# Performance work log

Measured on AMD Instinct MI355X. Metric: run time of the kernel, lower is better.

Reference implementation:

```python
import jax, jax.numpy as jnp
import numpy as np

W = 8          # window_size (small/key side)
WU = 2 * W     # window_size_up (big/query side)
H = 4          # num_heads
SF = 128       # sf_dim
BF = 256       # bf_dim
HD = SF // H   # head_dim = 32
SCALE = HD ** -0.5
TABLE = (2 * WU - 1) * (2 * W - 1)  # 465


def _relative_position_index():
    # big coords (2, WU*WU), small coords (2, W*W), 'ij' meshgrid like torch
    ch, cw = jnp.meshgrid(jnp.arange(WU), jnp.arange(WU), indexing='ij')
    big = jnp.stack([ch.reshape(-1), cw.reshape(-1)])          # (2, Nb)
    sh, sw = jnp.meshgrid(jnp.arange(W), jnp.arange(W), indexing='ij')
    small = jnp.stack([sh.reshape(-1), sw.reshape(-1)])        # (2, Ns)
    rel = big[:, :, None] - small[:, None, :]                  # (2, Nb, Ns)
    idx = (rel[0] + W - 1) * (2 * W - 1) + (rel[1] + W - 1)    # (Nb, Ns)
    return idx


def setup_inputs() -> dict:
    key = jax.random.key(0)
    ks = jax.random.split(key, 9)
    B_ = 1024
    Nb, Ns = WU * WU, W * W
    inp = {
        'big_x': jax.random.normal(ks[0], (B_, Nb, BF), jnp.float32),
        'small_x': jax.random.normal(ks[1], (B_, Ns, SF), jnp.float32),
        # proj1: bf_dim -> sf_dim
        'W1': jax.random.normal(ks[2], (BF, SF), jnp.float32) * (BF ** -0.5),
        'b1': jnp.zeros((SF,), jnp.float32),
        # fused qkv: sf_dim -> 3*sf_dim
        'Wqkv': jax.random.normal(ks[3], (SF, 3 * SF), jnp.float32) * (SF ** -0.5),
        'bqkv': jnp.zeros((3 * SF,), jnp.float32),
        # proj2: sf_dim -> bf_dim
        'W2': jax.random.normal(ks[4], (SF, BF), jnp.float32) * (SF ** -0.5),
        'b2': jnp.zeros((BF,), jnp.float32),
        # relative position bias table, trunc_normal std=0.02
        'bias_table': jax.random.normal(ks[5], (TABLE, H), jnp.float32) * 0.02,
    }
    return inp


def reference(big_x, small_x, W1, b1, Wqkv, bqkv, W2, b2, bias_table):
    B_, Nb, _ = big_x.shape
    Ns = small_x.shape[1]

    big = big_x @ W1 + b1                                      # (B, Nb, SF)

    # only q of big and k,v of small are used downstream
    qb = (big @ Wqkv[:, :SF] + bqkv[:SF]).reshape(B_, Nb, H, HD)
    ks_ = (small_x @ Wqkv[:, SF:2 * SF] + bqkv[SF:2 * SF]).reshape(B_, Ns, H, HD)
    vs = (small_x @ Wqkv[:, 2 * SF:] + bqkv[2 * SF:]).reshape(B_, Ns, H, HD)

    attn = jnp.einsum('bqhd,bkhd->bhqk', qb * SCALE, ks_)      # (B, H, Nb, Ns)

    idx = _relative_position_index()                           # (Nb, Ns)
    bias = bias_table[idx]                                     # (Nb, Ns, H)
    attn = attn + jnp.transpose(bias, (2, 0, 1))[None]         # broadcast over B

    attn = jax.nn.softmax(attn, axis=-1)
    out = jnp.einsum('bhqk,bkhd->bqhd', attn, vs).reshape(B_, Nb, SF)
    return out @ W2 + b2                                       # (B, Nb, BF)
```

## Files before the change

kernel.cpp:

```cpp
#include <hip/hip_runtime.h>
#include <stdint.h>

#define NH      4
#define SF      128
#define BF      256
#define HD      32
#define NB      256
#define NS      64
#define NBATCH  1024

typedef short bf16x8 __attribute__((ext_vector_type(8)));
typedef float f32x4  __attribute__((ext_vector_type(4)));

#define WEFFT_OFF 0
#define BEFF_OFF  65536
#define WKVT_OFF  66048
#define W2T_OFF   131584
#define BMATT_OFF 197120

#define LDS_SK  0
#define LDS_SVT 16384
#define LDS_SQ  32768
#define LDS_TOTAL 65536

__device__ __forceinline__ short f2b(float x){
  uint32_t u = __float_as_uint(x);
  u += 0x7fff + ((u >> 16) & 1);
  return (short)(u >> 16);
}
__device__ __forceinline__ uint32_t cvt_pk_bf16(float lo, float hi){
  uint32_t r;
  asm("v_cvt_pk_bf16_f32 %0, %1, %2" : "=v"(r) : "v"(lo), "v"(hi));
  return r;
}
__device__ __forceinline__ int swz256(int row, int byteInRow){
  return row * 256 + (byteInRow ^ ((row & 7) << 4));
}
__device__ __forceinline__ int swz128(int row, int byteInRow){
  return row * 128 + (byteInRow ^ ((row & 7) << 4));
}

__global__ void cowin_prep(const float* __restrict__ W1, const float* __restrict__ b1,
                           const float* __restrict__ Wqkv, const float* __restrict__ bqkv,
                           const float* __restrict__ W2, const float* __restrict__ tbl,
                           void* ws)
{
  short* weffT = (short*)((char*)ws + WEFFT_OFF);
  float* beff  = (float*)((char*)ws + BEFF_OFF);
  short* wkvT  = (short*)((char*)ws + WKVT_OFF);
  short* w2T   = (short*)((char*)ws + W2T_OFF);
  float* bmatT = (float*)((char*)ws + BMATT_OFF);
  const float L2E = 1.4426950408889634f;
  const float QS  = 0.17677669529663687f * L2E;

  int bid = blockIdx.x, t = threadIdx.x;
  if (bid < 128){
    int n = bid, k = t;
    float acc = 0.f;
    for (int c = 0; c < SF; ++c) acc += W1[k * SF + c] * Wqkv[c * (3*SF) + n];
    weffT[n * 256 + k] = f2b(acc * QS);
  } else if (bid == 128){
    if (t < 128){
      int n = t;
      float acc = bqkv[n];
      for (int c = 0; c < SF; ++c) acc += b1[c] * Wqkv[c * (3*SF) + n];
      beff[n] = acc * QS;
    }
  } else if (bid < 145){
    int base = (bid - 129) * 2048 + t * 8;
    for (int j = 0; j < 8; ++j){
      int i = base + j, n = i >> 7, k = i & 127;
      wkvT[i] = f2b(Wqkv[k * (3*SF) + SF + n]);
    }
  } else if (bid < 161){
    int base = (bid - 145) * 2048 + t * 8;
    for (int j = 0; j < 8; ++j){
      int i = base + j, n = i >> 7, k = i & 127;
      w2T[i] = f2b(W2[k * BF + n]);
    }
  } else {
    int i = (bid - 161) * 256 + t;
    int h = i >> 14, kk = (i >> 8) & 63, q = i & 255;
    int qh = q >> 4, qw = q & 15, kh = kk >> 3, kw = kk & 7;
    int idx = (qh - kh + 7) * 15 + (qw - kw + 7);
    bmatT[i] = tbl[idx * 4 + h] * L2E;
  }
}

__global__ __launch_bounds__(512, 4) void cowin_main(
    const float* __restrict__ big_x, const float* __restrict__ small_x,
    const float* __restrict__ bqkv,  const float* __restrict__ b2,
    const void* __restrict__ ws, float* __restrict__ out)
{
  extern __shared__ char smem[];
  const short* weffT = (const short*)((const char*)ws + WEFFT_OFF);
  const float* beff  = (const float*)((const char*)ws + BEFF_OFF);
  const short* wkvT  = (const short*)((const char*)ws + WKVT_OFF);
  const short* w2T   = (const short*)((const char*)ws + W2T_OFF);
  const float* bmatT = (const float*)((const char*)ws + BMATT_OFF);

  const int bid = blockIdx.x;
  const int b  = bid >> 1;
  const int hf = bid & 1;
  const int t    = threadIdx.x;
  const int w    = t >> 6;
  const int lane = t & 63;
  const int li   = lane & 15;
  const int g    = lane >> 4;

  const f32x4 vzero = {0.f, 0.f, 0.f, 0.f};

  const float* bx = big_x + (size_t)b * NB * BF + (size_t)hf * 128 * BF;
  const int qrow = t >> 2, qq = (t & 3) * 16;

  float4 ld[4];
  {
    const float* sx = small_x + (size_t)b * (NS * SF);
    int tok = t >> 3, p = t & 7;
    const float4* src = (const float4*)(sx + tok * SF + p * 16);
    float4 sv[4];
    #pragma unroll
    for (int j = 0; j < 4; ++j) sv[j] = src[j];
    {
      const float4* s_ = (const float4*)(bx + qrow * BF + qq);
      #pragma unroll
      for (int j = 0; j < 4; ++j) ld[j] = s_[j];
    }
    uint32_t pk[8];
    #pragma unroll
    for (int j = 0; j < 4; ++j){
      pk[2*j]   = cvt_pk_bf16(sv[j].x, sv[j].y);
      pk[2*j+1] = cvt_pk_bf16(sv[j].z, sv[j].w);
    }
    #pragma unroll
    for (int c = 0; c < 2; ++c){
      uint4 u; u.x = pk[c*4]; u.y = pk[c*4+1]; u.z = pk[c*4+2]; u.w = pk[c*4+3];
      *(uint4*)(smem + LDS_SK + swz256(tok, p * 32 + c * 16)) = u;
    }
  }
  __syncthreads();

  f32x4 kv[4][2];
  #pragma unroll
  for (int m = 0; m < 4; ++m){ kv[m][0] = vzero; kv[m][1] = vzero; }

  #pragma unroll
  for (int ks = 0; ks < 4; ++ks){
    bf16x8 afr[4];
    #pragma unroll
    for (int m = 0; m < 4; ++m)
      afr[m] = *(const bf16x8*)(smem + LDS_SK + swz256(m*16 + li, (ks*32 + g*8) * 2));
    #pragma unroll
    for (int n2 = 0; n2 < 2; ++n2){
      int n = w * 32 + n2 * 16 + li;
      bf16x8 bfr = *(const bf16x8*)(wkvT + n * 128 + ks * 32 + g * 8);
      #pragma unroll
      for (int m = 0; m < 4; ++m)
        kv[m][n2] = __builtin_amdgcn_mfma_f32_16x16x32_bf16(afr[m], bfr, kv[m][n2], 0, 0, 0);
    }
  }
  __syncthreads();

  if (w < 4){
    #pragma unroll
    for (int n2 = 0; n2 < 2; ++n2){
      int feat = w * 32 + n2 * 16 + li;
      float bias = bqkv[SF + feat];
      #pragma unroll
      for (int m = 0; m < 4; ++m){
        f32x4 vv = kv[m][n2];
        uint32_t p0 = cvt_pk_bf16(vv[0] + bias, vv[1] + bias);
        uint32_t p1 = cvt_pk_bf16(vv[2] + bias, vv[3] + bias);
        int tok0 = m * 16 + g * 4;
        *(short*)(smem + LDS_SK + swz256(tok0 + 0, feat * 2)) = (short)(p0);
        *(short*)(smem + LDS_SK + swz256(tok0 + 1, feat * 2)) = (short)(p0 >> 16);
        *(short*)(smem + LDS_SK + swz256(tok0 + 2, feat * 2)) = (short)(p1);
        *(short*)(smem + LDS_SK + swz256(tok0 + 3, feat * 2)) = (short)(p1 >> 16);
      }
    }
  } else {
    #pragma unroll
    for (int n2 = 0; n2 < 2; ++n2){
      int feat = (w - 4) * 32 + n2 * 16 + li;
      float bias = bqkv[2 * SF + feat];
      #pragma unroll
      for (int m = 0; m < 4; ++m){
        f32x4 vv = kv[m][n2];
        uint2 u;
        u.x = cvt_pk_bf16(vv[0] + bias, vv[1] + bias);
        u.y = cvt_pk_bf16(vv[2] + bias, vv[3] + bias);
        *(uint2*)(smem + LDS_SVT + swz128(feat, (m * 16 + g * 4) * 2)) = u;
      }
    }
  }

  f32x4 qacc[8];
  #pragma unroll
  for (int m = 0; m < 8; ++m) qacc[m] = vzero;

  {
    uint32_t pk[8];
    #pragma unroll
    for (int j = 0; j < 4; ++j){
      pk[2*j]   = cvt_pk_bf16(ld[j].x, ld[j].y);
      pk[2*j+1] = cvt_pk_bf16(ld[j].z, ld[j].w);
    }
    char* buf0 = smem + LDS_SQ;
    #pragma unroll
    for (int c = 0; c < 2; ++c){
      uint4 u; u.x = pk[c*4]; u.y = pk[c*4+1]; u.z = pk[c*4+2]; u.w = pk[c*4+3];
      *(uint4*)(buf0 + swz128(qrow, qq * 2 + c * 16)) = u;
    }
    const float4* s_ = (const float4*)(bx + qrow * BF + 64 + qq);
    #pragma unroll
    for (int j = 0; j < 4; ++j) ld[j] = s_[j];
  }

  for (int kc = 0; kc < 4; ++kc){
    __syncthreads();
    if (kc < 3){
      uint32_t pk[8];
      #pragma unroll
      for (int j = 0; j < 4; ++j){
        pk[2*j]   = cvt_pk_bf16(ld[j].x, ld[j].y);
        pk[2*j+1] = cvt_pk_bf16(ld[j].z, ld[j].w);
      }
      char* bufn = smem + LDS_SQ + ((kc + 1) & 1) * 16384;
      #pragma unroll
      for (int c = 0; c < 2; ++c){
        uint4 u; u.x = pk[c*4]; u.y = pk[c*4+1]; u.z = pk[c*4+2]; u.w = pk[c*4+3];
        *(uint4*)(bufn + swz128(qrow, qq * 2 + c * 16)) = u;
      }
      if (kc < 2){
        const float4* s_ = (const float4*)(bx + qrow * BF + (kc + 2) * 64 + qq);
        #pragma unroll
        for (int j = 0; j < 4; ++j) ld[j] = s_[j];
      }
    }
    const char* buf = smem + LDS_SQ + (kc & 1) * 16384;
    const int n = w * 16 + li;
    #pragma unroll
    for (int ks = 0; ks < 2; ++ks){
      bf16x8 afr[8];
      #pragma unroll
      for (int m = 0; m < 8; ++m)
        afr[m] = *(const bf16x8*)(buf + swz128(m*16 + li, (ks*32 + g*8) * 2));
      bf16x8 bfr = *(const bf16x8*)(weffT + n * 256 + kc * 64 + ks * 32 + g * 8);
      #pragma unroll
      for (int m = 0; m < 8; ++m)
        qacc[m] = __builtin_amdgcn_mfma_f32_16x16x32_bf16(afr[m], bfr, qacc[m], 0, 0, 0);
    }
  }
  __syncthreads();

  {
    int feat = w * 16 + li;
    float be = beff[feat];
    #pragma unroll
    for (int m = 0; m < 8; ++m){
      f32x4 vv = qacc[m];
      uint32_t p0 = cvt_pk_bf16(vv[0] + be, vv[1] + be);
      uint32_t p1 = cvt_pk_bf16(vv[2] + be, vv[3] + be);
      int r0 = m * 16 + g * 4;
      *(short*)(smem + LDS_SQ + swz256(r0 + 0, feat * 2)) = (short)(p0);
      *(short*)(smem + LDS_SQ + swz256(r0 + 1, feat * 2)) = (short)(p0 >> 16);
      *(short*)(smem + LDS_SQ + swz256(r0 + 2, feat * 2)) = (short)(p1);
      *(short*)(smem + LDS_SQ + swz256(r0 + 3, feat * 2)) = (short)(p1 >> 16);
    }
  }
  __syncthreads();

  const int h  = w & 3;
  const int qh = w >> 2;
  f32x4 sacc[4][4];
  #pragma unroll
  for (int m = 0; m < 4; ++m)
    #pragma unroll
    for (int n = 0; n < 4; ++n) sacc[m][n] = vzero;
  {
    bf16x8 afr[4];
    #pragma unroll
    for (int m = 0; m < 4; ++m)
      afr[m] = *(const bf16x8*)(smem + LDS_SK + swz256(m*16 + li, (h*32 + g*8) * 2));
    #pragma unroll
    for (int n = 0; n < 4; ++n){
      bf16x8 bfr = *(const bf16x8*)(smem + LDS_SQ + swz256(qh*64 + n*16 + li, (h*32 + g*8) * 2));
      #pragma unroll
      for (int m = 0; m < 4; ++m)
        sacc[m][n] = __builtin_amdgcn_mfma_f32_16x16x32_bf16(afr[m], bfr, sacc[m][n], 0, 0, 0);
    }
  }
  __syncthreads();

  {
    const float* bm = bmatT + h * (64 * 256);
    #pragma unroll
    for (int m = 0; m < 4; ++m){
      #pragma unroll
      for (int n = 0; n < 4; ++n){
        int qg = hf * 128 + qh * 64 + n * 16 + li;
        #pragma unroll
        for (int r = 0; r < 4; ++r){
          int key = m * 16 + g * 4 + r;
          sacc[m][n][r] += bm[key * 256 + qg];
        }
      }
    }
  }

  float sm[4];
  #pragma unroll
  for (int n = 0; n < 4; ++n){
    float mx = sacc[0][n][0];
    #pragma unroll
    for (int m = 0; m < 4; ++m)
      #pragma unroll
      for (int r = 0; r < 4; ++r) mx = fmaxf(mx, sacc[m][n][r]);
    mx = fmaxf(mx, __shfl_xor(mx, 16));
    mx = fmaxf(mx, __shfl_xor(mx, 32));
    float s0 = 0.f;
    #pragma unroll
    for (int m = 0; m < 4; ++m)
      #pragma unroll
      for (int r = 0; r < 4; ++r){
        float e = __builtin_amdgcn_exp2f(sacc[m][n][r] - mx);
        sacc[m][n][r] = e;
        s0 += e;
      }
    s0 += __shfl_xor(s0, 16);
    s0 += __shfl_xor(s0, 32);
    sm[n] = __builtin_amdgcn_rcpf(s0);
  }

  f32x4 oacc[2][2][2];
  #pragma unroll
  for (int hl = 0; hl < 2; ++hl)
    #pragma unroll
    for (int m2 = 0; m2 < 2; ++m2)
      #pragma unroll
      for (int n4 = 0; n4 < 2; ++n4) oacc[hl][m2][n4] = vzero;

  char* sp = smem + LDS_SQ + w * 4096;
  #pragma unroll
  for (int hl = 0; hl < 2; ++hl){
    #pragma unroll
    for (int n4 = 0; n4 < 2; ++n4){
      int n = hl * 2 + n4;
      #pragma unroll
      for (int m = 0; m < 4; ++m){
        uint2 u;
        u.x = cvt_pk_bf16(sacc[m][n][0], sacc[m][n][1]);
        u.y = cvt_pk_bf16(sacc[m][n][2], sacc[m][n][3]);
        *(uint2*)(sp + swz128(n4 * 16 + li, (m * 16 + g * 4) * 2)) = u;
      }
    }
    #pragma unroll
    for (int kk = 0; kk < 2; ++kk){
      bf16x8 afr[2];
      #pragma unroll
      for (int m2 = 0; m2 < 2; ++m2)
        afr[m2] = *(const bf16x8*)(smem + LDS_SVT + swz128(h*32 + m2*16 + li, (kk*32 + g*8) * 2));
      #pragma unroll
      for (int n4 = 0; n4 < 2; ++n4){
        bf16x8 bfr = *(const bf16x8*)(sp + swz128(n4 * 16 + li, (kk*32 + g*8) * 2));
        #pragma unroll
        for (int m2 = 0; m2 < 2; ++m2)
          oacc[hl][m2][n4] = __builtin_amdgcn_mfma_f32_16x16x32_bf16(afr[m2], bfr, oacc[hl][m2][n4], 0, 0, 0);
      }
    }
  }
  __syncthreads();

  #pragma unroll
  for (int hl = 0; hl < 2; ++hl)
    #pragma unroll
    for (int m2 = 0; m2 < 2; ++m2)
      #pragma unroll
      for (int n4 = 0; n4 < 2; ++n4){
        float rs = sm[hl * 2 + n4];
        f32x4 vv = oacc[hl][m2][n4];
        uint2 u;
        u.x = cvt_pk_bf16(vv[0] * rs, vv[1] * rs);
        u.y = cvt_pk_bf16(vv[2] * rs, vv[3] * rs);
        int q = qh * 64 + hl * 32 + n4 * 16 + li;
        *(uint2*)(smem + swz256(q, (h*32 + m2*16 + g*4) * 2)) = u;
      }
  __syncthreads();

  f32x4 facc[8][2];
  #pragma unroll
  for (int m = 0; m < 8; ++m){ facc[m][0] = vzero; facc[m][1] = vzero; }

  #pragma unroll
  for (int kc = 0; kc < 4; ++kc){
    bf16x8 afr[8];
    #pragma unroll
    for (int m = 0; m < 8; ++m)
      afr[m] = *(const bf16x8*)(smem + swz256(m*16 + li, (kc*32 + g*8) * 2));
    #pragma unroll
    for (int nt = 0; nt < 2; ++nt){
      int n = w * 32 + nt * 16 + li;
      bf16x8 bfr = *(const bf16x8*)(w2T + n * 128 + kc * 32 + g * 8);
      #pragma unroll
      for (int m = 0; m < 8; ++m)
        facc[m][nt] = __builtin_amdgcn_mfma_f32_16x16x32_bf16(afr[m], bfr, facc[m][nt], 0, 0, 0);
    }
  }

  float* op = out + (size_t)b * NB * BF + (size_t)hf * 128 * BF;
  #pragma unroll
  for (int nt = 0; nt < 2; ++nt){
    int col = w * 32 + nt * 16 + li;
    float bb = b2[col];
    #pragma unroll
    for (int m = 0; m < 8; ++m){
      int r0 = m * 16 + g * 4;
      #pragma unroll
      for (int r = 0; r < 4; ++r)
        op[(size_t)(r0 + r) * BF + col] = facc[m][nt][r] + bb;
    }
  }
}

extern "C" void kernel_launch(void* const* d_in, const int* in_sizes, int n_in,
                              void* d_out, int out_size, void* d_ws, size_t ws_size,
                              hipStream_t stream)
{
  const float* big_x   = (const float*)d_in[0];
  const float* small_x = (const float*)d_in[1];
  const float* W1      = (const float*)d_in[2];
  const float* b1      = (const float*)d_in[3];
  const float* Wqkv    = (const float*)d_in[4];
  const float* bqkv    = (const float*)d_in[5];
  const float* W2      = (const float*)d_in[6];
  const float* b2      = (const float*)d_in[7];
  const float* tbl     = (const float*)d_in[8];
  float* out = (float*)d_out;

  (void)in_sizes; (void)n_in; (void)out_size; (void)ws_size;

  cowin_prep<<<417, 256, 0, stream>>>(W1, b1, Wqkv, bqkv, W2, tbl, d_ws);

  hipFuncSetAttribute(reinterpret_cast<const void*>(cowin_main),
                      hipFuncAttributeMaxDynamicSharedMemorySize, LDS_TOTAL);
  cowin_main<<<NBATCH * 2, 512, LDS_TOTAL, stream>>>(big_x, small_x, bqkv, b2, d_ws, out);
}
```

Before: 179.3 us.

## Make workgroups persistent over four half-batches with cross-iteration prefetch and transposed MFMAs

The grid shrinks from 2048 to 512 workgroups, each looping over two batches and both query halves. K/V projections are computed once per batch and reused across both halves. The next tile's big_x and small_x loads are issued early so they overlap compute, and the blockIdx-to-batch mapping is swizzled. Several GEMMs swap operand roles so outputs and biases are written as contiguous float4 vectors, and the bias matrix layout is transposed for vector loads. The tradeoff is fewer workgroups (less parallelism, possible tail imbalance) and higher register pressure.

Result: slower. 331.8 us (+85.0%).

```diff
diff --git a/kernel.cpp b/kernel.cpp
--- a/kernel.cpp
+++ b/kernel.cpp
@@ -20,7 +20,7 @@
 
 #define LDS_SK  0
 #define LDS_SVT 16384
-#define LDS_SQ  32768
+#define LDS_R3  32768
 #define LDS_TOTAL 65536
 
 __device__ __forceinline__ short f2b(float x){
@@ -80,8 +80,8 @@
     }
   } else {
     int i = (bid - 161) * 256 + t;
-    int h = i >> 14, kk = (i >> 8) & 63, q = i & 255;
-    int qh = q >> 4, qw = q & 15, kh = kk >> 3, kw = kk & 7;
+    int h = i >> 14, q = (i >> 6) & 255, key = i & 63;
+    int qh = q >> 4, qw = q & 15, kh = key >> 3, kw = key & 7;
     int idx = (qh - kh + 7) * 15 + (qw - kw + 7);
     bmatT[i] = tbl[idx * 4 + h] * L2E;
   }
@@ -99,325 +99,347 @@
   const short* w2T   = (const short*)((const char*)ws + W2T_OFF);
   const float* bmatT = (const float*)((const char*)ws + BMATT_OFF);
 
-  const int bid = blockIdx.x;
-  const int b  = bid >> 1;
-  const int hf = bid & 1;
+  const int wg  = blockIdx.x;
+  const int swz = (wg & 7) * 64 + (wg >> 3);
   const int t    = threadIdx.x;
   const int w    = t >> 6;
   const int lane = t & 63;
   const int li   = lane & 15;
   const int g    = lane >> 4;
+  const int h  = w & 3;
+  const int qh = w >> 2;
 
   const f32x4 vzero = {0.f, 0.f, 0.f, 0.f};
 
-  const float* bx = big_x + (size_t)b * NB * BF + (size_t)hf * 128 * BF;
+  const int tok = t >> 3, p = t & 7;
   const int qrow = t >> 2, qq = (t & 3) * 16;
 
-  float4 ld[4];
+  float4 sv[4], ld[4];
   {
-    const float* sx = small_x + (size_t)b * (NS * SF);
-    int tok = t >> 3, p = t & 7;
-    const float4* src = (const float4*)(sx + tok * SF + p * 16);
-    float4 sv[4];
-    #pragma unroll
-    for (int j = 0; j < 4; ++j) sv[j] = src[j];
-    {
-      const float4* s_ = (const float4*)(bx + qrow * BF + qq);
-      #pragma unroll
-      for (int j = 0; j < 4; ++j) ld[j] = s_[j];
-    }
-    uint32_t pk[8];
-    #pragma unroll
-    for (int j = 0; j < 4; ++j){
-      pk[2*j]   = cvt_pk_bf16(sv[j].x, sv[j].y);
-      pk[2*j+1] = cvt_pk_bf16(sv[j].z, sv[j].w);
-    }
-    #pragma unroll
-    for (int c = 0; c < 2; ++c){
-      uint4 u; u.x = pk[c*4]; u.y = pk[c*4+1]; u.z = pk[c*4+2]; u.w = pk[c*4+3];
-      *(uint4*)(smem + LDS_SK + swz256(tok, p * 32 + c * 16)) = u;
-    }
+    int b0 = swz * 2;
+    const float* sx = small_x + (size_t)b0 * (NS * SF);
+    const float4* s0 = (const float4*)(sx + tok * SF + p * 16);
+    #pragma unroll
+    for (int i = 0; i < 4; ++i) sv[i] = s0[i];
+    const float* bx0 = big_x + (size_t)b0 * NB * BF;
+    const float4* s1 = (const float4*)(bx0 + qrow * BF + qq);
+    #pragma unroll
+    for (int i = 0; i < 4; ++i) ld[i] = s1[i];
   }
-  __syncthreads();
-
-  f32x4 kv[4][2];
-  #pragma unroll
-  for (int m = 0; m < 4; ++m){ kv[m][0] = vzero; kv[m][1] = vzero; }
-
-  #pragma unroll
-  for (int ks = 0; ks < 4; ++ks){
-    bf16x8 afr[4];
-    #pragma unroll
-    for (int m = 0; m < 4; ++m)
-      afr[m] = *(const bf16x8*)(smem + LDS_SK + swz256(m*16 + li, (ks*32 + g*8) * 2));
-    #pragma unroll
-    for (int n2 = 0; n2 < 2; ++n2){
-      int n = w * 32 + n2 * 16 + li;
-      bf16x8 bfr = *(const bf16x8*)(wkvT + n * 128 + ks * 32 + g * 8);
-      #pragma unroll
-      for (int m = 0; m < 4; ++m)
-        kv[m][n2] = __builtin_amdgcn_mfma_f32_16x16x32_bf16(afr[m], bfr, kv[m][n2], 0, 0, 0);
-    }
-  }
-  __syncthreads();
-
-  if (w < 4){
-    #pragma unroll
-    for (int n2 = 0; n2 < 2; ++n2){
-      int feat = w * 32 + n2 * 16 + li;
-      float bias = bqkv[SF + feat];
-      #pragma unroll
-      for (int m = 0; m < 4; ++m){
-        f32x4 vv = kv[m][n2];
-        uint32_t p0 = cvt_pk_bf16(vv[0] + bias, vv[1] + bias);
-        uint32_t p1 = cvt_pk_bf16(vv[2] + bias, vv[3] + bias);
-        int tok0 = m * 16 + g * 4;
-        *(short*)(smem + LDS_SK + swz256(tok0 + 0, feat * 2)) = (short)(p0);
-        *(short*)(smem + LDS_SK + swz256(tok0 + 1, feat * 2)) = (short)(p0 >> 16);
-        *(short*)(smem + LDS_SK + swz256(tok0 + 2, feat * 2)) = (short)(p1);
-        *(short*)(smem + LDS_SK + swz256(tok0 + 3, feat * 2)) = (short)(p1 >> 16);
-      }
-    }
-  } else {
-    #pragma unroll
-    for (int n2 = 0; n2 < 2; ++n2){
-      int feat = (w - 4) * 32 + n2 * 16 + li;
-      float bias = bqkv[2 * SF + feat];
-      #pragma unroll
-      for (int m = 0; m < 4; ++m){
-        f32x4 vv = kv[m][n2];
-        uint2 u;
-        u.x = cvt_pk_bf16(vv[0] + bias, vv[1] + bias);
-        u.y = cvt_pk_bf16(vv[2] + bias, vv[3] + bias);
-        *(uint2*)(smem + LDS_SVT + swz128(feat, (m * 16 + g * 4) * 2)) = u;
-      }
-    }
-  }
-
-  f32x4 qacc[8];
-  #pragma unroll
-  for (int m = 0; m < 8; ++m) qacc[m] = vzero;
-
-  {
-    uint32_t pk[8];
-    #pragma unroll
-    for (int j = 0; j < 4; ++j){
-      pk[2*j]   = cvt_pk_bf16(ld[j].x, ld[j].y);
-      pk[2*j+1] = cvt_pk_bf16(ld[j].z, ld[j].w);
-    }
-    char* buf0 = smem + LDS_SQ;
-    #pragma unroll
-    for (int c = 0; c < 2; ++c){
-      uint4 u; u.x = pk[c*4]; u.y = pk[c*4+1]; u.z = pk[c*4+2]; u.w = pk[c*4+3];
-      *(uint4*)(buf0 + swz128(qrow, qq * 2 + c * 16)) = u;
-    }
-    const float4* s_ = (const float4*)(bx + qrow * BF + 64 + qq);
-    #pragma unroll
-    for (int j = 0; j < 4; ++j) ld[j] = s_[j];
-  }
-
-  for (int kc = 0; kc < 4; ++kc){
-    __syncthreads();
-    if (kc < 3){
+
+  for (int j = 0; j < 4; ++j){
+    const int b  = swz * 2 + (j >> 1);
+    const int hf = j & 1;
+    const float* bx = big_x + (size_t)b * NB * BF + (size_t)hf * 128 * BF;
+
+    __syncthreads();
+
+    if (hf == 0){
       uint32_t pk[8];
       #pragma unroll
-      for (int j = 0; j < 4; ++j){
-        pk[2*j]   = cvt_pk_bf16(ld[j].x, ld[j].y);
-        pk[2*j+1] = cvt_pk_bf16(ld[j].z, ld[j].w);
-      }
-      char* bufn = smem + LDS_SQ + ((kc + 1) & 1) * 16384;
+      for (int i = 0; i < 4; ++i){
+        pk[2*i]   = cvt_pk_bf16(sv[i].x, sv[i].y);
+        pk[2*i+1] = cvt_pk_bf16(sv[i].z, sv[i].w);
+      }
       #pragma unroll
       for (int c = 0; c < 2; ++c){
         uint4 u; u.x = pk[c*4]; u.y = pk[c*4+1]; u.z = pk[c*4+2]; u.w = pk[c*4+3];
-        *(uint4*)(bufn + swz128(qrow, qq * 2 + c * 16)) = u;
-      }
-      if (kc < 2){
-        const float4* s_ = (const float4*)(bx + qrow * BF + (kc + 2) * 64 + qq);
-        #pragma unroll
-        for (int j = 0; j < 4; ++j) ld[j] = s_[j];
-      }
-    }
-    const char* buf = smem + LDS_SQ + (kc & 1) * 16384;
-    const int n = w * 16 + li;
-    #pragma unroll
-    for (int ks = 0; ks < 2; ++ks){
-      bf16x8 afr[8];
-      #pragma unroll
-      for (int m = 0; m < 8; ++m)
-        afr[m] = *(const bf16x8*)(buf + swz128(m*16 + li, (ks*32 + g*8) * 2));
-      bf16x8 bfr = *(const bf16x8*)(weffT + n * 256 + kc * 64 + ks * 32 + g * 8);
-      #pragma unroll
-      for (int m = 0; m < 8; ++m)
-        qacc[m] = __builtin_amdgcn_mfma_f32_16x16x32_bf16(afr[m], bfr, qacc[m], 0, 0, 0);
-    }
-  }
-  __syncthreads();
-
-  {
-    int feat = w * 16 + li;
-    float be = beff[feat];
-    #pragma unroll
-    for (int m = 0; m < 8; ++m){
-      f32x4 vv = qacc[m];
-      uint32_t p0 = cvt_pk_bf16(vv[0] + be, vv[1] + be);
-      uint32_t p1 = cvt_pk_bf16(vv[2] + be, vv[3] + be);
-      int r0 = m * 16 + g * 4;
-      *(short*)(smem + LDS_SQ + swz256(r0 + 0, feat * 2)) = (short)(p0);
-      *(short*)(smem + LDS_SQ + swz256(r0 + 1, feat * 2)) = (short)(p0 >> 16);
-      *(short*)(smem + LDS_SQ + swz256(r0 + 2, feat * 2)) = (short)(p1);
-      *(short*)(smem + LDS_SQ + swz256(r0 + 3, feat * 2)) = (short)(p1 >> 16);
-    }
-  }
-  __syncthreads();
-
-  const int h  = w & 3;
-  const int qh = w >> 2;
-  f32x4 sacc[4][4];
-  #pragma unroll
-  for (int m = 0; m < 4; ++m)
-    #pragma unroll
-    for (int n = 0; n < 4; ++n) sacc[m][n] = vzero;
-  {
-    bf16x8 afr[4];
+        *(uint4*)(smem + LDS_SK + swz256(tok, p * 32 + c * 16)) = u;
+      }
+    }
+    {
+      uint32_t pk[8];
+      #pragma unroll
+      for (int i = 0; i < 4; ++i){
+        pk[2*i]   = cvt_pk_bf16(ld[i].x, ld[i].y);
+        pk[2*i+1] = cvt_pk_bf16(ld[i].z, ld[i].w);
+      }
+      #pragma unroll
+      for (int c = 0; c < 2; ++c){
+        uint4 u; u.x = pk[c*4]; u.y = pk[c*4+1]; u.z = pk[c*4+2]; u.w = pk[c*4+3];
+        *(uint4*)(smem + LDS_R3 + swz128(qrow, qq * 2 + c * 16)) = u;
+      }
+      const float4* s_ = (const float4*)(bx + qrow * BF + 64 + qq);
+      #pragma unroll
+      for (int i = 0; i < 4; ++i) ld[i] = s_[i];
+    }
+    __syncthreads();
+
+    if (hf == 0){
+      f32x4 kv8[8];
+      #pragma unroll
+      for (int i = 0; i < 8; ++i) kv8[i] = vzero;
+
+      if (w < 4){
+        #pragma unroll
+        for (int ks = 0; ks < 4; ++ks){
+          bf16x8 a2[2];
+          #pragma unroll
+          for (int mf = 0; mf < 2; ++mf)
+            a2[mf] = *(const bf16x8*)(wkvT + (w*32 + mf*16 + li) * 128 + ks*32 + g*8);
+          #pragma unroll
+          for (int n4 = 0; n4 < 4; ++n4){
+            bf16x8 b4 = *(const bf16x8*)(smem + LDS_SK + swz256(n4*16 + li, (ks*32 + g*8) * 2));
+            #pragma unroll
+            for (int mf = 0; mf < 2; ++mf)
+              kv8[mf*4+n4] = __builtin_amdgcn_mfma_f32_16x16x32_bf16(a2[mf], b4, kv8[mf*4+n4], 0, 0, 0);
+          }
+        }
+      } else {
+        #pragma unroll
+        for (int ks = 0; ks < 4; ++ks){
+          bf16x8 afr[4];
+          #pragma unroll
+          for (int m = 0; m < 4; ++m)
+            afr[m] = *(const bf16x8*)(smem + LDS_SK + swz256(m*16 + li, (ks*32 + g*8) * 2));
+          #pragma unroll
+          for (int n2 = 0; n2 < 2; ++n2){
+            int n = w * 32 + n2 * 16 + li;
+            bf16x8 bfr = *(const bf16x8*)(wkvT + n * 128 + ks*32 + g*8);
+            #pragma unroll
+            for (int m = 0; m < 4; ++m)
+              kv8[m*2+n2] = __builtin_amdgcn_mfma_f32_16x16x32_bf16(afr[m], bfr, kv8[m*2+n2], 0, 0, 0);
+          }
+        }
+      }
+      __syncthreads();
+
+      if (w < 4){
+        #pragma unroll
+        for (int mf = 0; mf < 2; ++mf){
+          int f0 = w*32 + mf*16 + g*4;
+          f32x4 bb = *(const f32x4*)(bqkv + SF + f0);
+          #pragma unroll
+          for (int n4 = 0; n4 < 4; ++n4){
+            f32x4 vv = kv8[mf*4+n4];
+            uint2 u;
+            u.x = cvt_pk_bf16(vv[0] + bb[0], vv[1] + bb[1]);
+            u.y = cvt_pk_bf16(vv[2] + bb[2], vv[3] + bb[3]);
+            *(uint2*)(smem + LDS_SK + swz256(n4*16 + li, f0 * 2)) = u;
+          }
+        }
+      } else {
+        #pragma unroll
+        for (int n2 = 0; n2 < 2; ++n2){
+          int feat = (w-4)*32 + n2*16 + li;
+          float bias = bqkv[2*SF + feat];
+          #pragma unroll
+          for (int m = 0; m < 4; ++m){
+            f32x4 vv = kv8[m*2+n2];
+            uint2 u;
+            u.x = cvt_pk_bf16(vv[0] + bias, vv[1] + bias);
+            u.y = cvt_pk_bf16(vv[2] + bias, vv[3] + bias);
+            *(uint2*)(smem + LDS_SVT + swz128(feat, (m*16 + g*4) * 2)) = u;
+          }
+        }
+      }
+    }
+
+    f32x4 qacc[8];
+    #pragma unroll
+    for (int m = 0; m < 8; ++m) qacc[m] = vzero;
+
+    for (int kc = 0; kc < 4; ++kc){
+      __syncthreads();
+      if (kc < 3){
+        uint32_t pk[8];
+        #pragma unroll
+        for (int i = 0; i < 4; ++i){
+          pk[2*i]   = cvt_pk_bf16(ld[i].x, ld[i].y);
+          pk[2*i+1] = cvt_pk_bf16(ld[i].z, ld[i].w);
+        }
+        char* bufn = smem + LDS_R3 + ((kc + 1) & 1) * 16384;
+        #pragma unroll
+        for (int c = 0; c < 2; ++c){
+          uint4 u; u.x = pk[c*4]; u.y = pk[c*4+1]; u.z = pk[c*4+2]; u.w = pk[c*4+3];
+          *(uint4*)(bufn + swz128(qrow, qq * 2 + c * 16)) = u;
+        }
+        if (kc < 2){
+          const float4* s_ = (const float4*)(bx + qrow * BF + (kc + 2) * 64 + qq);
+          #pragma unroll
+          for (int i = 0; i < 4; ++i) ld[i] = s_[i];
+        }
+      } else if (j == 1){
+        const float* sx2 = small_x + (size_t)(swz * 2 + 1) * (NS * SF);
+        const float4* s0 = (const float4*)(sx2 + tok * SF + p * 16);
+        #pragma unroll
+        for (int i = 0; i < 4; ++i) sv[i] = s0[i];
+      }
+      const char* buf = smem + LDS_R3 + (kc & 1) * 16384;
+      #pragma unroll
+      for (int ks = 0; ks < 2; ++ks){
+        bf16x8 a = *(const bf16x8*)(weffT + (w*16 + li) * 256 + kc*64 + ks*32 + g*8);
+        #pragma unroll
+        for (int nt = 0; nt < 8; ++nt){
+          bf16x8 bq = *(const bf16x8*)(buf + swz128(nt*16 + li, (ks*32 + g*8) * 2));
+          qacc[nt] = __builtin_amdgcn_mfma_f32_16x16x32_bf16(a, bq, qacc[nt], 0, 0, 0);
+        }
+      }
+    }
+    __syncthreads();
+
+    {
+      f32x4 be = *(const f32x4*)(beff + w*16 + g*4);
+      #pragma unroll
+      for (int nt = 0; nt < 8; ++nt){
+        f32x4 vv = qacc[nt];
+        uint2 u;
+        u.x = cvt_pk_bf16(vv[0] + be[0], vv[1] + be[1]);
+        u.y = cvt_pk_bf16(vv[2] + be[2], vv[3] + be[3]);
+        *(uint2*)(smem + LDS_R3 + swz256(nt*16 + li, (w*16 + g*4) * 2)) = u;
+      }
+    }
+    __syncthreads();
+
+    f32x4 sacc[4][4];
     #pragma unroll
     for (int m = 0; m < 4; ++m)
-      afr[m] = *(const bf16x8*)(smem + LDS_SK + swz256(m*16 + li, (h*32 + g*8) * 2));
+      #pragma unroll
+      for (int n = 0; n < 4; ++n) sacc[m][n] = vzero;
+    {
+      bf16x8 afr[4];
+      #pragma unroll
+      for (int m = 0; m < 4; ++m)
+        afr[m] = *(const bf16x8*)(smem + LDS_SK + swz256(m*16 + li, (h*32 + g*8) * 2));
+      #pragma unroll
+      for (int n = 0; n < 4; ++n){
+        bf16x8 bfr = *(const bf16x8*)(smem + LDS_R3 + swz256(qh*64 + n*16 + li, (h*32 + g*8) * 2));
+        #pragma unroll
+        for (int m = 0; m < 4; ++m)
+          sacc[m][n] = __builtin_amdgcn_mfma_f32_16x16x32_bf16(afr[m], bfr, sacc[m][n], 0, 0, 0);
+      }
+    }
+    __syncthreads();
+
     #pragma unroll
     for (int n = 0; n < 4; ++n){
-      bf16x8 bfr = *(const bf16x8*)(smem + LDS_SQ + swz256(qh*64 + n*16 + li, (h*32 + g*8) * 2));
+      const float* bm = bmatT + ((size_t)(h * 256 + hf*128 + qh*64 + n*16 + li)) * 64;
+      #pragma unroll
+      for (int m = 0; m < 4; ++m){
+        f32x4 bb = *(const f32x4*)(bm + m*16 + g*4);
+        sacc[m][n] += bb;
+      }
+    }
+
+    float sm[4];
+    #pragma unroll
+    for (int n = 0; n < 4; ++n){
+      float mx = sacc[0][n][0];
       #pragma unroll
       for (int m = 0; m < 4; ++m)
-        sacc[m][n] = __builtin_amdgcn_mfma_f32_16x16x32_bf16(afr[m], bfr, sacc[m][n], 0, 0, 0);
-    }
-  }
-  __syncthreads();
-
-  {
-    const float* bm = bmatT + h * (64 * 256);
-    #pragma unroll
-    for (int m = 0; m < 4; ++m){
-      #pragma unroll
-      for (int n = 0; n < 4; ++n){
-        int qg = hf * 128 + qh * 64 + n * 16 + li;
+        #pragma unroll
+        for (int r = 0; r < 4; ++r) mx = fmaxf(mx, sacc[m][n][r]);
+      mx = fmaxf(mx, __shfl_xor(mx, 16));
+      mx = fmaxf(mx, __shfl_xor(mx, 32));
+      float s0 = 0.f;
+      #pragma unroll
+      for (int m = 0; m < 4; ++m)
         #pragma unroll
         for (int r = 0; r < 4; ++r){
-          int key = m * 16 + g * 4 + r;
-          sacc[m][n][r] += bm[key * 256 + qg];
-        }
-      }
-    }
-  }
-
-  float sm[4];
-  #pragma unroll
-  for (int n = 0; n < 4; ++n){
-    float mx = sacc[0][n][0];
-    #pragma unroll
-    for (int m = 0; m < 4; ++m)
-      #pragma unroll
-      for (int r = 0; r < 4; ++r) mx = fmaxf(mx, sacc[m][n][r]);
-    mx = fmaxf(mx, __shfl_xor(mx, 16));
-    mx = fmaxf(mx, __shfl_xor(mx, 32));
-    float s0 = 0.f;
-    #pragma unroll
-    for (int m = 0; m < 4; ++m)
-      #pragma unroll
-      for (int r = 0; r < 4; ++r){
-        float e = __builtin_amdgcn_exp2f(sacc[m][n][r] - mx);
-        sacc[m][n][r] = e;
-        s0 += e;
-      }
-    s0 += __shfl_xor(s0, 16);
-    s0 += __shfl_xor(s0, 32);
-    sm[n] = __builtin_amdgcn_rcpf(s0);
-  }
-
-  f32x4 oacc[2][2][2];
-  #pragma unroll
-  for (int hl = 0; hl < 2; ++hl)
-    #pragma unroll
-    for (int m2 = 0; m2 < 2; ++m2)
-      #pragma unroll
-      for (int n4 = 0; n4 < 2; ++n4) oacc[hl][m2][n4] = vzero;
-
-  char* sp = smem + LDS_SQ + w * 4096;
-  #pragma unroll
-  for (int hl = 0; hl < 2; ++hl){
-    #pragma unroll
-    for (int n4 = 0; n4 < 2; ++n4){
-      int n = hl * 2 + n4;
-      #pragma unroll
-      for (int m = 0; m < 4; ++m){
-        uint2 u;
-        u.x = cvt_pk_bf16(sacc[m][n][0], sacc[m][n][1]);
-        u.y = cvt_pk_bf16(sacc[m][n][2], sacc[m][n][3]);
-        *(uint2*)(sp + swz128(n4 * 16 + li, (m * 16 + g * 4) * 2)) = u;
-      }
-    }
-    #pragma unroll
-    for (int kk = 0; kk < 2; ++kk){
-      bf16x8 afr[2];
+          float e = __builtin_amdgcn_exp2f(sacc[m][n][r] - mx);
+          sacc[m][n][r] = e;
+          s0 += e;
+        }
+      s0 += __shfl_xor(s0, 16);
+      s0 += __shfl_xor(s0, 32);
+      sm[n] = __builtin_amdgcn_rcpf(s0);
+    }
+
+    f32x4 oacc[2][2][2];
+    #pragma unroll
+    for (int hl = 0; hl < 2; ++hl)
       #pragma unroll
       for (int m2 = 0; m2 < 2; ++m2)
-        afr[m2] = *(const bf16x8*)(smem + LDS_SVT + swz128(h*32 + m2*16 + li, (kk*32 + g*8) * 2));
+        #pragma unroll
+        for (int n4 = 0; n4 < 2; ++n4) oacc[hl][m2][n4] = vzero;
+
+    char* sp = smem + LDS_R3 + w * 4096;
+    #pragma unroll
+    for (int hl = 0; hl < 2; ++hl){
       #pragma unroll
       for (int n4 = 0; n4 < 2; ++n4){
-        bf16x8 bfr = *(const bf16x8*)(sp + swz128(n4 * 16 + li, (kk*32 + g*8) * 2));
+        int n = hl * 2 + n4;
+        #pragma unroll
+        for (int m = 0; m < 4; ++m){
+          uint2 u;
+          u.x = cvt_pk_bf16(sacc[m][n][0], sacc[m][n][1]);
+          u.y = cvt_pk_bf16(sacc[m][n][2], sacc[m][n][3]);
+          *(uint2*)(sp + swz128(n4 * 16 + li, (m * 16 + g * 4) * 2)) = u;
+        }
+      }
+      #pragma unroll
+      for (int kk = 0; kk < 2; ++kk){
+        bf16x8 afr2[2];
         #pragma unroll
         for (int m2 = 0; m2 < 2; ++m2)
-          oacc[hl][m2][n4] = __builtin_amdgcn_mfma_f32_16x16x32_bf16(afr[m2], bfr, oacc[hl][m2][n4], 0, 0, 0);
-      }
-    }
-  }
-  __syncthreads();
-
-  #pragma unroll
-  for (int hl = 0; hl < 2; ++hl)
-    #pragma unroll
-    for (int m2 = 0; m2 < 2; ++m2)
-      #pragma unroll
-      for (int n4 = 0; n4 < 2; ++n4){
-        float rs = sm[hl * 2 + n4];
-        f32x4 vv = oacc[hl][m2][n4];
-        uint2 u;
-        u.x = cvt_pk_bf16(vv[0] * rs, vv[1] * rs);
-        u.y = cvt_pk_bf16(vv[2] * rs, vv[3] * rs);
-        int q = qh * 64 + hl * 32 + n4 * 16 + li;
-        *(uint2*)(smem + swz256(q, (h*32 + m2*16 + g*4) * 2)) = u;
-      }
-  __syncthreads();
-
-  f32x4 facc[8][2];
-  #pragma unroll
-  for (int m = 0; m < 8; ++m){ facc[m][0] = vzero; facc[m][1] = vzero; }
-
-  #pragma unroll
-  for (int kc = 0; kc < 4; ++kc){
-    bf16x8 afr[8];
-    #pragma unroll
-    for (int m = 0; m < 8; ++m)
-      afr[m] = *(const bf16x8*)(smem + swz256(m*16 + li, (kc*32 + g*8) * 2));
-    #pragma unroll
-    for (int nt = 0; nt < 2; ++nt){
-      int n = w * 32 + nt * 16 + li;
-      bf16x8 bfr = *(const bf16x8*)(w2T + n * 128 + kc * 32 + g * 8);
-      #pragma unroll
-      for (int m = 0; m < 8; ++m)
-        facc[m][nt] = __builtin_amdgcn_mfma_f32_16x16x32_bf16(afr[m], bfr, facc[m][nt], 0, 0, 0);
-    }
-  }
-
-  float* op = out + (size_t)b * NB * BF + (size_t)hf * 128 * BF;
-  #pragma unroll
-  for (int nt = 0; nt < 2; ++nt){
-    int col = w * 32 + nt * 16 + li;
-    float bb = b2[col];
-    #pragma unroll
-    for (int m = 0; m < 8; ++m){
-      int r0 = m * 16 + g * 4;
-      #pragma unroll
-      for (int r = 0; r < 4; ++r)
-        op[(size_t)(r0 + r) * BF + col] = facc[m][nt][r] + bb;
+          afr2[m2] = *(const bf16x8*)(smem + LDS_SVT + swz128(h*32 + m2*16 + li, (kk*32 + g*8) * 2));
+        #pragma unroll
+        for (int n4 = 0; n4 < 2; ++n4){
+          bf16x8 bfr = *(const bf16x8*)(sp + swz128(n4 * 16 + li, (kk*32 + g*8) * 2));
+          #pragma unroll
+          for (int m2 = 0; m2 < 2; ++m2)
+            oacc[hl][m2][n4] = __builtin_amdgcn_mfma_f32_16x16x32_bf16(afr2[m2], bfr, oacc[hl][m2][n4], 0, 0, 0);
+        }
+      }
+    }
+    __syncthreads();
+
+    #pragma unroll
+    for (int hl = 0; hl < 2; ++hl)
+      #pragma unroll
+      for (int m2 = 0; m2 < 2; ++m2)
+        #pragma unroll
+        for (int n4 = 0; n4 < 2; ++n4){
+          float rs = sm[hl * 2 + n4];
+          f32x4 vv = oacc[hl][m2][n4];
+          uint2 u;
+          u.x = cvt_pk_bf16(vv[0] * rs, vv[1] * rs);
+          u.y = cvt_pk_bf16(vv[2] * rs, vv[3] * rs);
+          int q = qh * 64 + hl * 32 + n4 * 16 + li;
+          *(uint2*)(smem + LDS_R3 + swz256(q, (h*32 + m2*16 + g*4) * 2)) = u;
+        }
+    __syncthreads();
+
+    if (j < 3){
+      int b2_ = swz * 2 + ((j + 1) >> 1);
+      int hf2 = (j + 1) & 1;
+      const float* bx2 = big_x + (size_t)b2_ * NB * BF + (size_t)hf2 * 128 * BF;
+      const float4* s1 = (const float4*)(bx2 + qrow * BF + qq);
+      #pragma unroll
+      for (int i = 0; i < 4; ++i) ld[i] = s1[i];
+    }
+
+    f32x4 facc[2][8];
+    #pragma unroll
+    for (int mo = 0; mo < 2; ++mo)
+      #pragma unroll
+      for (int nt = 0; nt < 8; ++nt) facc[mo][nt] = vzero;
+
+    #pragma unroll
+    for (int kc = 0; kc < 4; ++kc){
+      bf16x8 a2[2];
+      #pragma unroll
+      for (int mo = 0; mo < 2; ++mo)
+        a2[mo] = *(const bf16x8*)(w2T + (w*32 + mo*16 + li) * 128 + kc*32 + g*8);
+      #pragma unroll
+      for (int nt = 0; nt < 8; ++nt){
+        bf16x8 b8 = *(const bf16x8*)(smem + LDS_R3 + swz256(nt*16 + li, (kc*32 + g*8) * 2));
+        #pragma unroll
+        for (int mo = 0; mo < 2; ++mo)
+          facc[mo][nt] = __builtin_amdgcn_mfma_f32_16x16x32_bf16(a2[mo], b8, facc[mo][nt], 0, 0, 0);
+      }
+    }
+
+    float* op = out + (size_t)b * NB * BF + (size_t)hf * 128 * BF;
+    #pragma unroll
+    for (int mo = 0; mo < 2; ++mo){
+      int c0 = w*32 + mo*16 + g*4;
+      f32x4 bb = *(const f32x4*)(b2 + c0);
+      #pragma unroll
+      for (int nt = 0; nt < 8; ++nt){
+        f32x4 vv = facc[mo][nt] + bb;
+        *(f32x4*)(op + (size_t)(nt*16 + li) * BF + c0) = vv;
+      }
     }
   }
 }
@@ -443,5 +465,5 @@
 
   hipFuncSetAttribute(reinterpret_cast<const void*>(cowin_main),
                       hipFuncAttributeMaxDynamicSharedMemorySize, LDS_TOTAL);
-  cowin_main<<<NBATCH * 2, 512, LDS_TOTAL, stream>>>(big_x, small_x, bqkv, b2, d_ws, out);
-}
+  cowin_main<<<512, 512, LDS_TOTAL, stream>>>(big_x, small_x, bqkv, b2, d_ws, out);
+}
```
